# Kernel optimization log

Hardware: AMD Instinct MI355X
Metric: run time of the kernel (lower is better)

The kernel has to match this reference:

```python
import jax, jax.numpy as jnp
import numpy as np

B, T, C, H = 4, 2048, 1024, 16
D = C // H  # key_dim = 64


def setup_inputs() -> dict:
    key = jax.random.key(0)
    k1, k2, k3 = jax.random.split(key, 3)
    x = jax.random.normal(k1, (B, T, C), dtype=jnp.float32)
    w_attn = jax.random.normal(k2, (C, 3 * C), dtype=jnp.float32) * 0.02
    b_attn = jnp.zeros((3 * C,), dtype=jnp.float32)
    w_proj = jax.random.normal(k3, (C, C), dtype=jnp.float32) * 0.02
    b_proj = jnp.zeros((C,), dtype=jnp.float32)
    return {"x": x, "w_attn": w_attn, "b_attn": b_attn,
            "w_proj": w_proj, "b_proj": b_proj}


def reference(x, w_attn, b_attn, w_proj, b_proj):
    b, t, c = x.shape
    d = c // H
    qkv = jnp.einsum('btc,cf->btf', x, w_attn) + b_attn  # [B,T,3C]
    q, k, v = jnp.split(qkv, 3, axis=-1)
    # [B,T,C] -> [B,H,T,D]
    q = q.reshape(b, t, H, d).transpose(0, 2, 1, 3)
    k = k.reshape(b, t, H, d).transpose(0, 2, 1, 3)
    v = v.reshape(b, t, H, d).transpose(0, 2, 1, 3)
    att = jnp.einsum('bhqd,bhkd->bhqk', q, k) / jnp.sqrt(jnp.float32(d))
    att = jax.nn.softmax(att, axis=-1)  # non-causal, full attention
    # dropout layers are identity at inference (rate=0.0 config)
    y = jnp.einsum('bhqk,bhkd->bhqd', att, v)
    y = y.transpose(0, 2, 1, 3).reshape(b, t, c)
    return jnp.einsum('btc,cf->btf', y, w_proj) + b_proj
```

## Files before the change

kernel.cpp:

```cpp
#include <hip/hip_runtime.h>
#include <math.h>

#define BB 4
#define TT 2048
#define CC 1024
#define HH 16
#define F3 3072
#define NTOK (BB*TT)
#define KDIM 1024

typedef __attribute__((ext_vector_type(8))) short short8;
typedef __attribute__((ext_vector_type(8))) unsigned short ushort8;
typedef __attribute__((ext_vector_type(8))) _Float16 half8;
typedef __attribute__((ext_vector_type(4))) unsigned short ushort4v;
typedef __attribute__((ext_vector_type(4))) float float4v;

static __device__ __forceinline__ unsigned short f2bf(float x) {
    union { float f; unsigned u; } v; v.f = x;
    unsigned r = v.u + 0x7fffu + ((v.u >> 16) & 1u);
    return (unsigned short)(r >> 16);
}
static __device__ __forceinline__ float bf2f(unsigned short h) {
    union { unsigned u; float f; } v; v.u = ((unsigned)h) << 16;
    return v.f;
}
static __device__ __forceinline__ unsigned short f2h(float x) {
    union { _Float16 h; unsigned short u; } v; v.h = (_Float16)x; return v.u;
}

static __device__ __forceinline__ void async16(const void* g, void* l) {
    __builtin_amdgcn_global_load_lds(
        (const __attribute__((address_space(1))) unsigned int*)g,
        (__attribute__((address_space(3))) unsigned int*)l, 16, 0, 0);
}

template <int C>
static __device__ __forceinline__ float dppf(float x) {
    return __int_as_float(
        __builtin_amdgcn_update_dpp(0, __float_as_int(x), C, 0xf, 0xf, true));
}
static __device__ __forceinline__ float red16_sum(float v) {
    v += dppf<0x128>(v);
    v += dppf<0x124>(v);
    v += dppf<0x4E>(v);
    v += dppf<0xB1>(v);
    return v;
}

#if __has_builtin(__builtin_amdgcn_exp2f)
#define EXP2(x) __builtin_amdgcn_exp2f(x)
#else
#define EXP2(x) __expf((x) * 0.6931471805599453f)
#endif

#define BAR()  asm volatile("s_barrier" ::: "memory")
#define VMW(n) asm volatile("s_waitcnt vmcnt(" #n ")" ::: "memory")

__global__ __launch_bounds__(256) void prep_w(
    const float* __restrict__ W, unsigned short* __restrict__ WtH,
    unsigned short* __restrict__ WtL, int N)
{
    __shared__ float Ls[64][65];
    const int t = threadIdx.x;
    const int n0 = blockIdx.x * 64, k0 = blockIdx.y * 64;
    const int cc = t & 63, rr = t >> 6;
    #pragma unroll
    for (int i = 0; i < 16; ++i) {
        const int row = rr + 4 * i;
        Ls[row][cc] = W[(long)(k0 + row) * N + n0 + cc];
    }
    __syncthreads();
    const int n = t >> 2, seg = (t & 3) << 4;
    ushort8 h0, h1, l0, l1;
    #pragma unroll
    for (int j = 0; j < 8; ++j) {
        float x0 = Ls[seg + j][n];
        h0[j] = f2bf(x0); l0[j] = f2bf(x0 - bf2f(h0[j]));
        float x1 = Ls[seg + 8 + j][n];
        h1[j] = f2bf(x1); l1[j] = f2bf(x1 - bf2f(h1[j]));
    }
    const long o = (long)(n0 + n) * KDIM + k0 + seg;
    *(ushort8*)(WtH + o) = h0;     *(ushort8*)(WtH + o + 8) = h1;
    *(ushort8*)(WtL + o) = l0;     *(ushort8*)(WtL + o + 8) = l1;
}

__global__ __launch_bounds__(256) void prep_w16(
    const float* __restrict__ W, unsigned short* __restrict__ WtF, int N)
{
    __shared__ float Ls[64][65];
    const int t = threadIdx.x;
    const int n0 = blockIdx.x * 64, k0 = blockIdx.y * 64;
    const int cc = t & 63, rr = t >> 6;
    #pragma unroll
    for (int i = 0; i < 16; ++i) {
        const int row = rr + 4 * i;
        Ls[row][cc] = W[(long)(k0 + row) * N + n0 + cc];
    }
    __syncthreads();
    const int n = t >> 2, seg = (t & 3) << 4;
    ushort8 h0, h1;
    #pragma unroll
    for (int j = 0; j < 8; ++j) {
        h0[j] = f2h(Ls[seg + j][n]);
        h1[j] = f2h(Ls[seg + 8 + j][n]);
    }
    const long o = (long)(n0 + n) * KDIM + k0 + seg;
    *(ushort8*)(WtF + o) = h0;     *(ushort8*)(WtF + o + 8) = h1;
}

__global__ __launch_bounds__(256) void split16(
    const float* __restrict__ X, unsigned short* __restrict__ XF)
{
    const long i = (long)blockIdx.x * 256 + threadIdx.x;
    const float4 v = ((const float4*)X)[i];
    ushort4v h;
    h[0] = f2h(v.x); h[1] = f2h(v.y); h[2] = f2h(v.z); h[3] = f2h(v.w);
    ((ushort4v*)XF)[i] = h;
}

__global__ __launch_bounds__(256) void gemm16_qkv(
    const unsigned short* __restrict__ A, const unsigned short* __restrict__ B,
    const float* __restrict__ bias, unsigned short* __restrict__ qkvp,
    unsigned short* __restrict__ VTp)
{
    __shared__ __align__(16) unsigned short sA[128 * 32];
    __shared__ __align__(16) unsigned short sB[128 * 32];

    const int tid = threadIdx.x;
    const int n0 = blockIdx.x * 128, m0 = blockIdx.y * 128;
    const int lane = tid & 63, w = tid >> 6;
    const int wm = w >> 1, wn = w & 1;
    const int l = lane & 15, quad = lane >> 4;

    unsigned short* const sbuf = (w < 2) ? sA : sB;
    const unsigned short* const gsrc = (w < 2) ? A + (long)m0 * KDIM
                                               : B + (long)n0 * KDIM;
    const int lrow = (w & 1) * 64 + (lane >> 2);
    const int lseg = ((lane & 3) - (lane >> 3)) & 3;
    const unsigned short* const gbase = gsrc + (long)lrow * KDIM + lseg * 8;
    unsigned short* const lbase = sbuf + (w & 1) * 2048 + lane * 8;

    const int swz = ((quad + (l >> 1)) & 3) * 8;

    float4v acc[4][4];
    #pragma unroll
    for (int mt = 0; mt < 4; ++mt)
        #pragma unroll
        for (int nt = 0; nt < 4; ++nt)
            acc[mt][nt] = (float4v){0.f, 0.f, 0.f, 0.f};

    for (int k0 = 0; k0 < KDIM; k0 += 32) {
        #pragma unroll
        for (int i = 0; i < 4; ++i)
            async16(gbase + (long)i * 16 * KDIM + k0, lbase + i * 512);
        __syncthreads();

        half8 fa[4];
        #pragma unroll
        for (int mt = 0; mt < 4; ++mt)
            fa[mt] = *(const half8*)&sA[(wm * 64 + mt * 16 + l) * 32 + swz];
        #pragma unroll
        for (int nt = 0; nt < 4; ++nt) {
            const half8 fb = *(const half8*)&sB[(wn * 64 + nt * 16 + l) * 32 + swz];
            #pragma unroll
            for (int mt = 0; mt < 4; ++mt)
                acc[mt][nt] = __builtin_amdgcn_mfma_f32_16x16x32_f16(fa[mt], fb, acc[mt][nt], 0, 0, 0);
        }
        __syncthreads();
    }

    #pragma unroll
    for (int nt = 0; nt < 4; ++nt) {
        const int col = n0 + wn * 64 + nt * 16 + l;
        const float bv = bias[col];
        if (col < 2048) {
            const float sc = (col < 1024) ? 0.18033688011112042f : 1.0f;
            #pragma unroll
            for (int mt = 0; mt < 4; ++mt)
                #pragma unroll
                for (int i = 0; i < 4; ++i) {
                    const long row = m0 + wm * 64 + mt * 16 + quad * 4 + i;
                    qkvp[row * F3 + col] = f2h((acc[mt][nt][i] + bv) * sc);
                }
        } else {
            const int d = col & 63;
            const int hh = (col >> 6) - 32;
            const int bb = m0 >> 11;
            const long vtoff = ((long)(bb * HH + hh) * 64 + d) * TT;
            #pragma unroll
            for (int mt = 0; mt < 4; ++mt) {
                const int t0 = (m0 & 2047) + wm * 64 + mt * 16 + quad * 4;
                ushort4v pk;
                #pragma unroll
                for (int i = 0; i < 4; ++i) pk[i] = f2bf(acc[mt][nt][i] + bv);
                *(ushort4v*)(VTp + vtoff + t0) = pk;
            }
        }
    }
}

__global__ __launch_bounds__(256) void gemm_split(
    const unsigned short* __restrict__ AH, const unsigned short* __restrict__ AL,
    const unsigned short* __restrict__ BH, const unsigned short* __restrict__ BL,
    const float* __restrict__ bias, void* __restrict__ outp,
    unsigned short* __restrict__ VTp, int N, int mode)
{
    __shared__ __align__(16) unsigned short sAH[128 * 32];
    __shared__ __align__(16) unsigned short sAL[128 * 32];
    __shared__ __align__(16) unsigned short sBH[128 * 32];
    __shared__ __align__(16) unsigned short sBL[128 * 32];

    const int tid = threadIdx.x;
    const int n0 = blockIdx.x * 128, m0 = blockIdx.y * 128;
    const int lane = tid & 63, w = tid >> 6;
    const int wm = w >> 1, wn = w & 1;
    const int l = lane & 15, quad = lane >> 4;

    unsigned short* const sbuf = (w == 0) ? sAH : (w == 1) ? sAL
                               : (w == 2) ? sBH : sBL;
    const unsigned short* const gsrc =
        (w == 0) ? AH + (long)m0 * KDIM : (w == 1) ? AL + (long)m0 * KDIM
      : (w == 2) ? BH + (long)n0 * KDIM : BL + (long)n0 * KDIM;
    const int lrow = lane >> 2;
    const int lseg = ((lane & 3) - (lane >> 3)) & 3;
    const unsigned short* const gbase = gsrc + (long)lrow * KDIM + lseg * 8;
    unsigned short* const lbase = sbuf + lane * 8;

    const int swz = ((quad + (l >> 1)) & 3) * 8;

    float4v acc[4][4];
    #pragma unroll
    for (int mt = 0; mt < 4; ++mt)
        #pragma unroll
        for (int nt = 0; nt < 4; ++nt)
            acc[mt][nt] = (float4v){0.f, 0.f, 0.f, 0.f};

    for (int k0 = 0; k0 < KDIM; k0 += 32) {
        #pragma unroll
        for (int i = 0; i < 8; ++i)
            async16(gbase + (long)i * 16 * KDIM + k0, lbase + i * 512);
        __syncthreads();

        short8 fah[4], fal[4];
        #pragma unroll
        for (int mt = 0; mt < 4; ++mt) {
            const int off = (wm * 64 + mt * 16 + l) * 32 + swz;
            fah[mt] = *(const short8*)&sAH[off];
            fal[mt] = *(const short8*)&sAL[off];
        }
        #pragma unroll
        for (int nt = 0; nt < 4; ++nt) {
            const int off = (wn * 64 + nt * 16 + l) * 32 + swz;
            const short8 fbh = *(const short8*)&sBH[off];
            const short8 fbl = *(const short8*)&sBL[off];
            #pragma unroll
            for (int mt = 0; mt < 4; ++mt) {
                acc[mt][nt] = __builtin_amdgcn_mfma_f32_16x16x32_bf16(fah[mt], fbh, acc[mt][nt], 0, 0, 0);
                acc[mt][nt] = __builtin_amdgcn_mfma_f32_16x16x32_bf16(fah[mt], fbl, acc[mt][nt], 0, 0, 0);
                acc[mt][nt] = __builtin_amdgcn_mfma_f32_16x16x32_bf16(fal[mt], fbh, acc[mt][nt], 0, 0, 0);
            }
        }
        __syncthreads();
    }

    #pragma unroll
    for (int nt = 0; nt < 4; ++nt) {
        const int col = n0 + wn * 64 + nt * 16 + l;
        const float bv = bias[col];
        #pragma unroll
        for (int mt = 0; mt < 4; ++mt)
            #pragma unroll
            for (int i = 0; i < 4; ++i) {
                const long row = m0 + wm * 64 + mt * 16 + quad * 4 + i;
                ((float*)outp)[row * N + col] = acc[mt][nt][i] + bv;
            }
    }
    (void)VTp; (void)mode;
}

#define STAGEKV(k0, bf) do { \
    async16(qkv + (base + (k0) + rK) * F3 + 1024 + hoff + sK * 8, &KV[bf][tid * 8]); \
    async16(VT + vtbase + (long)rK * TT + (k0) + sK * 8, &KV[2 + bf][tid * 8]); \
  } while (0)

#define ATTN_TILE(cur) do { \
    float4v sA[2][4]; \
    _Pragma("unroll") for (int qt = 0; qt < 2; ++qt) \
        _Pragma("unroll") for (int nt = 0; nt < 4; ++nt) \
            sA[qt][nt] = (float4v){0.f, 0.f, 0.f, 0.f}; \
     \
    __builtin_amdgcn_s_setprio(1); \
    _Pragma("unroll") for (int kit = 0; kit < 2; ++kit) { \
        const int seg = ((kit * 4 + quad) ^ xs) * 8; \
        _Pragma("unroll") for (int nt = 0; nt < 4; ++nt) { \
            const half8 kb = *(const half8*)&KV[cur][(16 * nt + l) * 64 + seg]; \
            sA[0][nt] = __builtin_amdgcn_mfma_f32_16x16x32_f16(qa[0][kit], kb, sA[0][nt], 0, 0, 0); \
            sA[1][nt] = __builtin_amdgcn_mfma_f32_16x16x32_f16(qa[1][kit], kb, sA[1][nt], 0, 0, 0); \
        } \
    } \
    __builtin_amdgcn_s_setprio(0); \
     \
    _Pragma("unroll") for (int qt = 0; qt < 2; ++qt) { \
        _Pragma("unroll") for (int nt = 0; nt < 4; ++nt) { \
            _Pragma("unroll") for (int i = 0; i < 4; ++i) { \
                const float p = EXP2(fminf(sA[qt][nt][i], 80.f)); \
                const unsigned pu = __float_as_uint(p); \
                l_part[qt][i] += __uint_as_float(pu & 0xFFFF0000u); \
                Ps[(wv * 32 + qt * 16 + quad * 4 + i) * 72 + 16 * nt + l] = \
                    (unsigned short)(pu >> 16); \
            } \
        } \
    } \
     \
    __builtin_amdgcn_s_setprio(1); \
    _Pragma("unroll") for (int kit = 0; kit < 2; ++kit) { \
        const short8 pa0 = *(const short8*)&Ps[(wv * 32 + l) * 72 + kit * 32 + quad * 8]; \
        const short8 pa1 = *(const short8*)&Ps[(wv * 32 + 16 + l) * 72 + kit * 32 + quad * 8]; \
        const int seg = ((kit * 4 + quad) ^ xs) * 8; \
        _Pragma("unroll") for (int dt = 0; dt < 4; ++dt) { \
            const short8 vb = *(const short8*)&KV[2 + cur][(16 * dt + l) * 64 + seg]; \
            acc[0][dt] = __builtin_amdgcn_mfma_f32_16x16x32_bf16(pa0, vb, acc[0][dt], 0, 0, 0); \
            acc[1][dt] = __builtin_amdgcn_mfma_f32_16x16x32_bf16(pa1, vb, acc[1][dt], 0, 0, 0); \
        } \
    } \
    __builtin_amdgcn_s_setprio(0); \
  } while (0)

__global__ __attribute__((amdgpu_flat_work_group_size(512, 512),
                          amdgpu_waves_per_eu(4)))
void attn_kernel(const unsigned short* __restrict__ qkv,
                 const unsigned short* __restrict__ VT,
                 unsigned short* __restrict__ yH,
                 unsigned short* __restrict__ yL)
{
    __shared__ __align__(16) unsigned short KV[4][64 * 64];
    __shared__ __align__(16) unsigned short Ps[256 * 72];

    const int tid = threadIdx.x;
    const int lid = blockIdx.x;
    const int work = (lid & 7) * 64 + (lid >> 3);
    const int q0 = (work & 7) * 256;
    const int bh = work >> 3;
    const int b = bh >> 4;
    const int hoff = (bh & 15) * 64;
    const long base = (long)(b * TT);
    const long vtbase = (long)bh * 64 * TT;

    const int lane = tid & 63;
    const int wv = tid >> 6;
    const int l = lane & 15;
    const int quad = lane >> 4;
    const int xs = l & 7;

    const int rK = tid >> 3;
    const int sK = (tid & 7) ^ (rK & 7);

    unsigned short* const KVf = &KV[0][0];

    #pragma unroll
    for (int i = 0; i < 4; ++i) {
        const int u = i * 512 + tid;
        const int r = u >> 3, s = (u & 7) ^ (r & 7);
        async16(qkv + (base + q0 + r) * F3 + hoff + s * 8, &KVf[u * 8]);
    }
    VMW(0); BAR();

    half8 qa[2][2];
    #pragma unroll
    for (int qt = 0; qt < 2; ++qt)
        #pragma unroll
        for (int kit = 0; kit < 2; ++kit) {
            const int seg = ((kit * 4 + quad) ^ xs) * 8;
            qa[qt][kit] = *(const half8*)&KVf[(wv * 32 + qt * 16 + l) * 64 + seg];
        }
    __syncthreads();

    float4v acc[2][4];
    float l_part[2][4];
    #pragma unroll
    for (int qt = 0; qt < 2; ++qt)
        #pragma unroll
        for (int dt = 0; dt < 4; ++dt) {
            acc[qt][dt] = (float4v){0.f, 0.f, 0.f, 0.f};
            l_part[qt][dt] = 0.f;
        }

    STAGEKV(0, 0);
    VMW(0); BAR();

    #pragma unroll 1
    for (int t = 0; t < TT / 64 - 1; ++t) {
        const int cur = t & 1;
        STAGEKV((t + 1) * 64, cur ^ 1);
        VMW(2);
        BAR();
        ATTN_TILE(cur);
        BAR();
    }
    VMW(0);
    BAR();
    ATTN_TILE(1);

    #pragma unroll
    for (int qt = 0; qt < 2; ++qt)
        #pragma unroll
        for (int i = 0; i < 4; ++i) {
            const float inv_l = 1.f / red16_sum(l_part[qt][i]);
            const long row = base + q0 + wv * 32 + qt * 16 + quad * 4 + i;
            #pragma unroll
            for (int dt = 0; dt < 4; ++dt) {
                const float o = acc[qt][dt][i] * inv_l;
                const unsigned short hh = f2bf(o);
                yH[row * CC + hoff + 16 * dt + l] = hh;
                yL[row * CC + hoff + 16 * dt + l] = f2bf(o - bf2f(hh));
            }
        }
}

extern "C" void kernel_launch(void* const* d_in, const int* in_sizes, int n_in,
                              void* d_out, int out_size, void* d_ws, size_t ws_size,
                              hipStream_t stream) {
    const float* x      = (const float*)d_in[0];
    const float* w_attn = (const float*)d_in[1];
    const float* b_attn = (const float*)d_in[2];
    const float* w_proj = (const float*)d_in[3];
    const float* b_proj = (const float*)d_in[4];
    float* out = (float*)d_out;

    char* wsb = (char*)d_ws;
    unsigned short* qkv = (unsigned short*)(wsb);
    unsigned short* VT  = (unsigned short*)(wsb + 50331648);
    unsigned short* xF  = (unsigned short*)(wsb + 67108864);
    unsigned short* yL  = (unsigned short*)(wsb + 83886080);
    unsigned short* WaF = (unsigned short*)(wsb + 100663296);
    unsigned short* WpH = (unsigned short*)(wsb + 106954752);
    unsigned short* WpL = (unsigned short*)(wsb + 109051904);

    prep_w16<<<dim3(F3 / 64, KDIM / 64), 256, 0, stream>>>(w_attn, WaF, F3);
    prep_w<<<dim3(CC / 64, KDIM / 64), 256, 0, stream>>>(w_proj, WpH, WpL, CC);
    split16<<<(NTOK * CC / 4) / 256, 256, 0, stream>>>(x, xF);

    gemm16_qkv<<<dim3(F3 / 128, NTOK / 128), 256, 0, stream>>>(
        xF, WaF, b_attn, qkv, VT);

    attn_kernel<<<dim3((TT / 256) * BB * HH), 512, 0, stream>>>(qkv, VT, xF, yL);

    gemm_split<<<dim3(CC / 128, NTOK / 128), 256, 0, stream>>>(
        xF, yL, WpH, WpL, b_proj, out, (unsigned short*)nullptr, CC, 0);
}
```

Before: 320.7 us.

## Double-buffer LDS tiles in QKV GEMM with async prefetch two stages ahead

Measured after the change: 319.9 us. About the same (-0.3%).

```diff
diff --git a/kernel.cpp b/kernel.cpp
--- a/kernel.cpp
+++ b/kernel.cpp
@@ -123,8 +123,8 @@
     const float* __restrict__ bias, unsigned short* __restrict__ qkvp,
     unsigned short* __restrict__ VTp)
 {
-    __shared__ __align__(16) unsigned short sA[128 * 32];
-    __shared__ __align__(16) unsigned short sB[128 * 32];
+    __shared__ __align__(16) unsigned short sA[2][128 * 32];
+    __shared__ __align__(16) unsigned short sB[2][128 * 32];
 
     const int tid = threadIdx.x;
     const int n0 = blockIdx.x * 128, m0 = blockIdx.y * 128;
@@ -132,15 +132,32 @@
     const int wm = w >> 1, wn = w & 1;
     const int l = lane & 15, quad = lane >> 4;
 
-    unsigned short* const sbuf = (w < 2) ? sA : sB;
-    const unsigned short* const gsrc = (w < 2) ? A + (long)m0 * KDIM
-                                               : B + (long)n0 * KDIM;
+    const int isB = (w >= 2);
+    const unsigned short* const gsrc = isB ? B + (long)n0 * KDIM
+                                           : A + (long)m0 * KDIM;
     const int lrow = (w & 1) * 64 + (lane >> 2);
     const int lseg = ((lane & 3) - (lane >> 3)) & 3;
     const unsigned short* const gbase = gsrc + (long)lrow * KDIM + lseg * 8;
-    unsigned short* const lbase = sbuf + (w & 1) * 2048 + lane * 8;
+    const int loff = (w & 1) * 2048 + lane * 8;
 
     const int swz = ((quad + (l >> 1)) & 3) * 8;
+
+#define STAGE16(buf, k0) do { \
+    unsigned short* const dst = (isB ? sB[buf] : sA[buf]) + loff; \
+    _Pragma("unroll") for (int i = 0; i < 4; ++i) \
+        async16(gbase + (long)i * 16 * KDIM + (k0), dst + i * 512); \
+  } while (0)
+
+#define COMP16(buf) do { \
+    half8 fa[4]; \
+    _Pragma("unroll") for (int mt = 0; mt < 4; ++mt) \
+        fa[mt] = *(const half8*)&sA[buf][(wm * 64 + mt * 16 + l) * 32 + swz]; \
+    _Pragma("unroll") for (int nt = 0; nt < 4; ++nt) { \
+        const half8 fb = *(const half8*)&sB[buf][(wn * 64 + nt * 16 + l) * 32 + swz]; \
+        _Pragma("unroll") for (int mt = 0; mt < 4; ++mt) \
+            acc[mt][nt] = __builtin_amdgcn_mfma_f32_16x16x32_f16(fa[mt], fb, acc[mt][nt], 0, 0, 0); \
+    } \
+  } while (0)
 
     float4v acc[4][4];
     #pragma unroll
@@ -149,25 +166,24 @@
         for (int nt = 0; nt < 4; ++nt)
             acc[mt][nt] = (float4v){0.f, 0.f, 0.f, 0.f};
 
-    for (int k0 = 0; k0 < KDIM; k0 += 32) {
-        #pragma unroll
-        for (int i = 0; i < 4; ++i)
-            async16(gbase + (long)i * 16 * KDIM + k0, lbase + i * 512);
-        __syncthreads();
-
-        half8 fa[4];
-        #pragma unroll
-        for (int mt = 0; mt < 4; ++mt)
-            fa[mt] = *(const half8*)&sA[(wm * 64 + mt * 16 + l) * 32 + swz];
-        #pragma unroll
-        for (int nt = 0; nt < 4; ++nt) {
-            const half8 fb = *(const half8*)&sB[(wn * 64 + nt * 16 + l) * 32 + swz];
-            #pragma unroll
-            for (int mt = 0; mt < 4; ++mt)
-                acc[mt][nt] = __builtin_amdgcn_mfma_f32_16x16x32_f16(fa[mt], fb, acc[mt][nt], 0, 0, 0);
-        }
-        __syncthreads();
-    }
+    STAGE16(0, 0);
+    STAGE16(1, 32);
+    VMW(4); BAR();
+
+    #pragma unroll 1
+    for (int t = 0; t < 30; ++t) {
+        const int cur = t & 1;
+        COMP16(cur);
+        BAR();
+        STAGE16(cur, (t + 2) * 32);
+        VMW(4); BAR();
+    }
+    COMP16(0);
+    BAR(); VMW(0); BAR();
+    COMP16(1);
+
+#undef STAGE16
+#undef COMP16
 
     #pragma unroll
     for (int nt = 0; nt < 4; ++nt) {
```
